# Kernel optimization log

Measured on AMD Instinct MI355X. Metric: run time of the kernel, lower is better.

## Reference

```python
import jax, jax.numpy as jnp
import numpy as np

B = 4096          # events
L = 524288        # total set points (avg 128 per event)
CIN = 16          # per-point feature size (set feature 'a')
DVEC = 32         # flat feature size (feature 'b')
PHI = [128, 128, 64]
MLP = [256, 128]
EPS = 1e-5        # BatchNorm1d eps


def setup_inputs() -> dict:
    key = jax.random.key(0)
    ks = jax.random.split(key, 10)
    def n(k, shape, scale=0.05):
        return jax.random.normal(k, shape, dtype=jnp.float32) * scale
    return {
        "x_a": jax.random.normal(ks[0], (1, CIN, L), dtype=jnp.float32),
        "x_b": jax.random.normal(ks[1], (B, DVEC), dtype=jnp.float32),
        # row 0 -> counts for set feature 'a'; row 1 ignored (Reshape branch)
        "sample_indices": jnp.full((2, B), L // B, dtype=jnp.int32),
        "W1": n(ks[2], (PHI[0], CIN)),  "b1": jnp.zeros((PHI[0],), jnp.float32),
        "W2": n(ks[3], (PHI[1], PHI[0])), "b2": jnp.zeros((PHI[1],), jnp.float32),
        "W3": n(ks[4], (PHI[2], PHI[1])), "b3": jnp.zeros((PHI[2],), jnp.float32),
        "Wm1": n(ks[5], (MLP[0], PHI[2] + DVEC)), "bm1": jnp.zeros((MLP[0],), jnp.float32),
        "g1": jnp.ones((MLP[0],), jnp.float32), "be1": jnp.zeros((MLP[0],), jnp.float32),
        "Wm2": n(ks[6], (MLP[1], MLP[0])), "bm2": jnp.zeros((MLP[1],), jnp.float32),
        "g2": jnp.ones((MLP[1],), jnp.float32), "be2": jnp.zeros((MLP[1],), jnp.float32),
        "Wm3": n(ks[7], (1, MLP[1])), "bm3": jnp.zeros((1,), jnp.float32),
    }


def _bn(x, g, b):
    # BatchNorm1d, training-mode batch stats, biased variance (torch semantics)
    mu = jnp.mean(x, axis=0)
    var = jnp.var(x, axis=0)
    return (x - mu) * jax.lax.rsqrt(var + EPS) * g + b


def reference(x_a, x_b, sample_indices,
              W1, b1, W2, b2, W3, b3,
              Wm1, bm1, g1, be1, Wm2, bm2, g2, be2, Wm3, bm3):
    counts = sample_indices[0].astype(jnp.int32)                       # [B]
    bounds = jnp.concatenate([jnp.zeros((1,), jnp.int32), jnp.cumsum(counts)])  # [B+1]

    # PhiNet: pointwise Conv1d stack (kernel size 1) on [CIN, L]
    h = x_a[0]
    h = jax.nn.relu(jnp.einsum('oc,cl->ol', W1, h) + b1[:, None])
    h = jax.nn.relu(jnp.einsum('oc,cl->ol', W2, h) + b2[:, None])
    h = jax.nn.relu(jnp.einsum('oc,cl->ol', W3, h) + b3[:, None])      # [64, L]

    # fused segment-mean: point p belongs to segment j iff bounds[j] <= p < bounds[j+1]
    seg = jnp.searchsorted(bounds, jnp.arange(h.shape[1], dtype=jnp.int32), side='right') - 1
    sums = jax.ops.segment_sum(h.T, seg, num_segments=counts.shape[0])  # [B, 64]
    means = sums / jnp.maximum(counts, 1).astype(jnp.float32)[:, None]

    # feature order: sorted keys -> ('a' set repr, 'b' flat)
    z = jnp.concatenate([means, x_b.reshape(-1, DVEC)], axis=1)        # [B, 96]

    z = jax.nn.relu(_bn(z @ Wm1.T + bm1, g1, be1))
    z = jax.nn.relu(_bn(z @ Wm2.T + bm2, g2, be2))
    return jax.nn.sigmoid(z @ Wm3.T + bm3)                             # [B, 1]
```

## Files before the change

kernel.cpp:

```cpp
#include <hip/hip_runtime.h>
#include <hip/hip_bf16.h>

#define B_EVENTS 4096
#define L_PTS    524288
#define CIN      16
#define C1       128
#define C2       128
#define C3       64
#define DVEC     32
#define ZDIM     96
#define M1       256
#define M2       128
#define BN_EPS   1e-5f
#define TPTS     64
#define EPB      4

typedef __attribute__((ext_vector_type(8))) short bf16x8;
typedef __attribute__((ext_vector_type(4))) float f32x4;

__device__ __forceinline__ ushort f2bf(float x) {
    union { float f; unsigned u; } a; a.f = x;
    unsigned r = (a.u + 0x7fffu + ((a.u >> 16) & 1u)) >> 16;
    return (ushort)r;
}

__device__ __forceinline__ unsigned cvtpk(float lo, float hi) {
    unsigned r;
    asm("v_cvt_pk_bf16_f32 %0, %1, %2" : "=v"(r) : "v"(lo), "v"(hi));
    return r;
}

__device__ __forceinline__ unsigned long long pack4relu(f32x4 a) {
    union { unsigned u[2]; unsigned long long ll; } pk;
    pk.u[0] = cvtpk(fmaxf(a[0], 0.f), fmaxf(a[1], 0.f));
    pk.u[1] = cvtpk(fmaxf(a[2], 0.f), fmaxf(a[3], 0.f));
    return pk.ll;
}

__device__ __forceinline__ int ldsoff(int base, int rowSlots, int c, int sir) {
    int s = c * rowSlots + sir;
    s ^= (c & 7);
    return base + s * 16;
}

__global__ __launch_bounds__(1024) void scan_zero_kernel(const int* __restrict__ si,
                                                         int* __restrict__ bounds,
                                                         float* __restrict__ stats) {
    __shared__ int sh[1024];
    const int tid = threadIdx.x;
    const int c0 = si[tid*4+0], c1 = si[tid*4+1], c2 = si[tid*4+2], c3 = si[tid*4+3];
    const int s4 = c0 + c1 + c2 + c3;
    sh[tid] = s4;
    if (tid < 768) stats[tid] = 0.f;
    __syncthreads();
    for (int off = 1; off < 1024; off <<= 1) {
        int add = (tid >= off) ? sh[tid - off] : 0;
        __syncthreads();
        sh[tid] += add;
        __syncthreads();
    }
    const int excl = (tid == 0) ? 0 : sh[tid - 1];
    bounds[tid*4+0] = excl;
    bounds[tid*4+1] = excl + c0;
    bounds[tid*4+2] = excl + c0 + c1;
    bounds[tid*4+3] = excl + c0 + c1 + c2;
    if (tid == 1023) bounds[B_EVENTS] = excl + s4;
}

__global__ __launch_bounds__(256) void prep_kernel(
    const float* __restrict__ W1, const float* __restrict__ W2, const float* __restrict__ W3,
    ushort* __restrict__ w1p, ushort* __restrict__ w2b, ushort* __restrict__ w3b)
{
    const int tid = blockIdx.x * 256 + threadIdx.x;
    const int nthr = gridDim.x * 256;
    for (int i = tid; i < C1 * 32; i += nthr) {
        const int r = i >> 5, k = i & 31;
        w1p[i] = (k < CIN) ? f2bf(W1[r * CIN + k]) : (ushort)0;
    }
    for (int i = tid; i < C2 * C1; i += nthr) w2b[i] = f2bf(W2[i]);
    for (int i = tid; i < C3 * C2; i += nthr) w3b[i] = f2bf(W3[i]);
}

__global__ __launch_bounds__(256, 2) void phi_mfma_kernel(
    const float* __restrict__ xa, const float* __restrict__ xb,
    const int* __restrict__ bounds,
    const ushort* __restrict__ w1p, const ushort* __restrict__ w2b, const ushort* __restrict__ w3b,
    const float* __restrict__ b1, const float* __restrict__ b2, const float* __restrict__ b3,
    float* __restrict__ z)
{
    __shared__ __align__(16) char lds[36864];
    __shared__ float msum[C3];

    const int tid  = threadIdx.x;
    const int lane = tid & 63;
    const int wid  = tid >> 6;
    const int wm   = wid >> 1;
    const int wn   = wid & 1;
    const int g4   = lane >> 4;
    const int c16  = lane & 15;

    bf16x8 a1[4], a2[4][4], a3[2][4];
    {
        const int r1 = wm * 64 + c16;
        #pragma unroll
        for (int mf = 0; mf < 4; ++mf)
            a1[mf] = *(const bf16x8*)&w1p[(r1 + mf * 16) * 32 + g4 * 8];
        #pragma unroll
        for (int mf = 0; mf < 4; ++mf)
            #pragma unroll
            for (int kf = 0; kf < 4; ++kf)
                a2[mf][kf] = *(const bf16x8*)&w2b[(r1 + mf * 16) * C1 + kf * 32 + g4 * 8];
        const int r3 = wm * 32 + c16;
        #pragma unroll
        for (int mf = 0; mf < 2; ++mf)
            #pragma unroll
            for (int kf = 0; kf < 4; ++kf)
                a3[mf][kf] = *(const bf16x8*)&w3b[(r3 + mf * 16) * C2 + kf * 32 + g4 * 8];
    }

    const int pt   = tid & 63;
    const int half = tid >> 6;
    const int xoff = ldsoff(0, 4, pt, half >> 1) + (half & 1) * 8;

    for (int e = 0; e < EPB; ++e) {
        const int j     = blockIdx.x * EPB + e;
        const int start = bounds[j];
        const int cnt   = bounds[j + 1] - start;

        if (tid < C3) msum[tid] = 0.f;

        float xr[4];
        #pragma unroll
        for (int jj = 0; jj < 4; ++jj)
            xr[jj] = (pt < cnt) ? xa[(size_t)(half * 4 + jj) * L_PTS + start + pt] : 0.f;
        {
            union { unsigned u[2]; unsigned long long ll; } pk;
            pk.u[0] = cvtpk(xr[0], xr[1]);
            pk.u[1] = cvtpk(xr[2], xr[3]);
            *(unsigned long long*)(lds + xoff) = pk.ll;
        }
        __syncthreads();

        for (int p0 = 0; p0 < cnt; p0 += TPTS) {
            const bool more = (p0 + TPTS) < cnt;

            if (more) {
                const int p = p0 + TPTS + pt;
                #pragma unroll
                for (int jj = 0; jj < 4; ++jj)
                    xr[jj] = (p < cnt) ? xa[(size_t)(half * 4 + jj) * L_PTS + start + p] : 0.f;
            }

            {
                f32x4 acc[4][2];
                #pragma unroll
                for (int mf = 0; mf < 4; ++mf) {
                    const f32x4 bb = *(const f32x4*)&b1[wm * 64 + mf * 16 + g4 * 4];
                    acc[mf][0] = bb; acc[mf][1] = bb;
                }
                bf16x8 bfrag[2];
                #pragma unroll
                for (int nf = 0; nf < 2; ++nf)
                    bfrag[nf] = *(const bf16x8*)(lds + ldsoff(0, 4, wn * 32 + nf * 16 + c16, g4));
                __builtin_amdgcn_s_setprio(1);
                #pragma unroll
                for (int nf = 0; nf < 2; ++nf)
                    #pragma unroll
                    for (int mf = 0; mf < 4; ++mf)
                        acc[mf][nf] = __builtin_amdgcn_mfma_f32_16x16x32_bf16(a1[mf], bfrag[nf], acc[mf][nf], 0, 0, 0);
                __builtin_amdgcn_s_setprio(0);
                #pragma unroll
                for (int mf = 0; mf < 4; ++mf)
                    #pragma unroll
                    for (int nf = 0; nf < 2; ++nf) {
                        const int c = wn * 32 + nf * 16 + c16;
                        const int sir = (wm * 64 + mf * 16) / 8 + (g4 >> 1);
                        *(unsigned long long*)(lds + ldsoff(4096, 16, c, sir) + (g4 & 1) * 8) = pack4relu(acc[mf][nf]);
                    }
            }
            __syncthreads();

            {
                f32x4 acc[4][2];
                #pragma unroll
                for (int mf = 0; mf < 4; ++mf) {
                    const f32x4 bb = *(const f32x4*)&b2[wm * 64 + mf * 16 + g4 * 4];
                    acc[mf][0] = bb; acc[mf][1] = bb;
                }
                #pragma unroll
                for (int nf = 0; nf < 2; ++nf) {
                    const int c = wn * 32 + nf * 16 + c16;
                    bf16x8 bk[4];
                    #pragma unroll
                    for (int kf = 0; kf < 4; ++kf)
                        bk[kf] = *(const bf16x8*)(lds + ldsoff(4096, 16, c, kf * 4 + g4));
                    __builtin_amdgcn_s_setprio(1);
                    #pragma unroll
                    for (int mf = 0; mf < 4; ++mf)
                        #pragma unroll
                        for (int kf = 0; kf < 4; ++kf)
                            acc[mf][nf] = __builtin_amdgcn_mfma_f32_16x16x32_bf16(a2[mf][kf], bk[kf], acc[mf][nf], 0, 0, 0);
                    __builtin_amdgcn_s_setprio(0);
                }
                #pragma unroll
                for (int mf = 0; mf < 4; ++mf)
                    #pragma unroll
                    for (int nf = 0; nf < 2; ++nf) {
                        const int c = wn * 32 + nf * 16 + c16;
                        const int sir = (wm * 64 + mf * 16) / 8 + (g4 >> 1);
                        *(unsigned long long*)(lds + ldsoff(20480, 16, c, sir) + (g4 & 1) * 8) = pack4relu(acc[mf][nf]);
                    }
            }
            __syncthreads();

            if (more) {
                union { unsigned u[2]; unsigned long long ll; } pk;
                pk.u[0] = cvtpk(xr[0], xr[1]);
                pk.u[1] = cvtpk(xr[2], xr[3]);
                *(unsigned long long*)(lds + xoff) = pk.ll;
            }

            {
                f32x4 acc3[2][2];
                #pragma unroll
                for (int mf = 0; mf < 2; ++mf) {
                    const f32x4 bb = *(const f32x4*)&b3[wm * 32 + mf * 16 + g4 * 4];
                    acc3[mf][0] = bb; acc3[mf][1] = bb;
                }
                #pragma unroll
                for (int nf = 0; nf < 2; ++nf) {
                    const int c = wn * 32 + nf * 16 + c16;
                    bf16x8 bk[4];
                    #pragma unroll
                    for (int kf = 0; kf < 4; ++kf)
                        bk[kf] = *(const bf16x8*)(lds + ldsoff(20480, 16, c, kf * 4 + g4));
                    __builtin_amdgcn_s_setprio(1);
                    #pragma unroll
                    for (int mf = 0; mf < 2; ++mf)
                        #pragma unroll
                        for (int kf = 0; kf < 4; ++kf)
                            acc3[mf][nf] = __builtin_amdgcn_mfma_f32_16x16x32_bf16(a3[mf][kf], bk[kf], acc3[mf][nf], 0, 0, 0);
                    __builtin_amdgcn_s_setprio(0);
                }
                float s[2][4];
                #pragma unroll
                for (int mf = 0; mf < 2; ++mf)
                    #pragma unroll
                    for (int r = 0; r < 4; ++r) s[mf][r] = 0.f;
                #pragma unroll
                for (int nf = 0; nf < 2; ++nf) {
                    const int col = p0 + wn * 32 + nf * 16 + c16;
                    const bool valid = col < cnt;
                    #pragma unroll
                    for (int mf = 0; mf < 2; ++mf)
                        #pragma unroll
                        for (int r = 0; r < 4; ++r) {
                            const float v = fmaxf(acc3[mf][nf][r], 0.f);
                            if (valid) s[mf][r] += v;
                        }
                }
                #pragma unroll
                for (int mf = 0; mf < 2; ++mf)
                    #pragma unroll
                    for (int r = 0; r < 4; ++r) {
                        float v = s[mf][r];
                        #pragma unroll
                        for (int m = 1; m < 16; m <<= 1) v += __shfl_xor(v, m, 64);
                        s[mf][r] = v;
                    }
                if (c16 == 0) {
                    #pragma unroll
                    for (int mf = 0; mf < 2; ++mf)
                        #pragma unroll
                        for (int r = 0; r < 4; ++r)
                            atomicAdd(&msum[wm * 32 + mf * 16 + g4 * 4 + r], s[mf][r]);
                }
            }
            __syncthreads();
        }

        if (tid < C3) {
            const float inv = 1.f / (float)max(cnt, 1);
            z[(size_t)j * ZDIM + tid] = msum[tid] * inv;
        } else if (tid < ZDIM) {
            z[(size_t)j * ZDIM + tid] = xb[(size_t)j * DVEC + (tid - C3)];
        }
    }
}

__global__ __launch_bounds__(256) void mlp1_kernel(
    const float* __restrict__ z, const float* __restrict__ Wm1, const float* __restrict__ bm1,
    float* __restrict__ y1, float* __restrict__ gsum, float* __restrict__ gsq)
{
    __shared__ float zs[16][ZDIM + 4];
    const int r0 = blockIdx.x * 16;
    const int tid = threadIdx.x;
    for (int i = tid; i < 16 * ZDIM; i += 256) {
        const int r = i / ZDIM, c = i - r * ZDIM;
        zs[r][c] = z[(size_t)(r0 + r) * ZDIM + c];
    }
    __syncthreads();
    const int o = tid;
    float acc[16];
    const float bb = bm1[o];
    #pragma unroll
    for (int r = 0; r < 16; ++r) acc[r] = bb;
    for (int c = 0; c < ZDIM; c += 4) {
        const float4 w = *(const float4*)&Wm1[o * ZDIM + c];
        #pragma unroll
        for (int r = 0; r < 16; ++r) {
            const float4 v = *(const float4*)&zs[r][c];
            acc[r] += w.x*v.x + w.y*v.y + w.z*v.z + w.w*v.w;
        }
    }
    float s = 0.f, sq = 0.f;
    #pragma unroll
    for (int r = 0; r < 16; ++r) {
        y1[(size_t)(r0 + r) * M1 + o] = acc[r];
        s += acc[r]; sq += acc[r] * acc[r];
    }
    atomicAdd(&gsum[o], s);
    atomicAdd(&gsq[o], sq);
}

__global__ void bnfin_kernel(const float* __restrict__ gsum, const float* __restrict__ gsq,
                             const float* __restrict__ g, const float* __restrict__ be,
                             float* __restrict__ scale, float* __restrict__ shift, int n)
{
    const int o = blockIdx.x * blockDim.x + threadIdx.x;
    if (o >= n) return;
    const float mu  = gsum[o] * (1.f / B_EVENTS);
    const float var = gsq[o] * (1.f / B_EVENTS) - mu * mu;
    const float rs  = rsqrtf(var + BN_EPS);
    const float sc  = rs * g[o];
    scale[o] = sc;
    shift[o] = be[o] - mu * sc;
}

__global__ __launch_bounds__(256) void mlp2_kernel(
    const float* __restrict__ y1, const float* __restrict__ scale1, const float* __restrict__ shift1,
    const float* __restrict__ Wm2, const float* __restrict__ bm2,
    float* __restrict__ y2, float* __restrict__ gsum, float* __restrict__ gsq)
{
    __shared__ float zs[16][M1 + 4];
    const int r0 = blockIdx.x * 16;
    const int tid = threadIdx.x;
    for (int i = tid; i < 16 * M1; i += 256) {
        const int r = i >> 8, c = i & (M1 - 1);
        const float v = y1[(size_t)(r0 + r) * M1 + c];
        zs[r][c] = fmaxf(v * scale1[c] + shift1[c], 0.f);
    }
    __syncthreads();
    const int o = tid & 127;
    const int h = tid >> 7;
    float acc[8];
    const float bb = bm2[o];
    #pragma unroll
    for (int r = 0; r < 8; ++r) acc[r] = bb;
    for (int c = 0; c < M1; c += 4) {
        const float4 w = *(const float4*)&Wm2[o * M1 + c];
        #pragma unroll
        for (int r = 0; r < 8; ++r) {
            const float4 v = *(const float4*)&zs[h * 8 + r][c];
            acc[r] += w.x*v.x + w.y*v.y + w.z*v.z + w.w*v.w;
        }
    }
    float s = 0.f, sq = 0.f;
    #pragma unroll
    for (int r = 0; r < 8; ++r) {
        y2[(size_t)(r0 + h * 8 + r) * M2 + o] = acc[r];
        s += acc[r]; sq += acc[r] * acc[r];
    }
    atomicAdd(&gsum[o], s);
    atomicAdd(&gsq[o], sq);
}

__global__ __launch_bounds__(256) void final_kernel(
    const float* __restrict__ y2, const float* __restrict__ scale2, const float* __restrict__ shift2,
    const float* __restrict__ Wm3, const float* __restrict__ bm3,
    float* __restrict__ out)
{
    const int tid = threadIdx.x;
    const int w = tid >> 6, l = tid & 63;
    const int r = blockIdx.x * 4 + w;
    const float e0 = fmaxf(y2[(size_t)r * M2 + l]      * scale2[l]      + shift2[l],      0.f);
    const float e1 = fmaxf(y2[(size_t)r * M2 + 64 + l] * scale2[64 + l] + shift2[64 + l], 0.f);
    float a = e0 * Wm3[l] + e1 * Wm3[64 + l];
    #pragma unroll
    for (int off = 32; off >= 1; off >>= 1) a += __shfl_down(a, off, 64);
    if (l == 0) out[r] = 1.f / (1.f + expf(-(a + bm3[0])));
}

extern "C" void kernel_launch(void* const* d_in, const int* in_sizes, int n_in,
                              void* d_out, int out_size, void* d_ws, size_t ws_size,
                              hipStream_t stream) {
    const float* xa  = (const float*)d_in[0];
    const float* xb  = (const float*)d_in[1];
    const int*   si  = (const int*)  d_in[2];
    const float* W1  = (const float*)d_in[3];
    const float* b1  = (const float*)d_in[4];
    const float* W2  = (const float*)d_in[5];
    const float* b2  = (const float*)d_in[6];
    const float* W3  = (const float*)d_in[7];
    const float* b3  = (const float*)d_in[8];
    const float* Wm1 = (const float*)d_in[9];
    const float* bm1 = (const float*)d_in[10];
    const float* g1  = (const float*)d_in[11];
    const float* be1 = (const float*)d_in[12];
    const float* Wm2 = (const float*)d_in[13];
    const float* bm2 = (const float*)d_in[14];
    const float* g2  = (const float*)d_in[15];
    const float* be2 = (const float*)d_in[16];
    const float* Wm3 = (const float*)d_in[17];
    const float* bm3 = (const float*)d_in[18];
    float* out = (float*)d_out;

    char* ws = (char*)d_ws;
    size_t off = 0;
    auto alloc = [&](size_t bytes) -> void* {
        void* p = ws + off;
        off = (off + bytes + 255) & ~(size_t)255;
        return p;
    };
    int*    bounds = (int*)   alloc((B_EVENTS + 1) * sizeof(int));
    float*  stats  = (float*) alloc(768 * sizeof(float));
    float*  z      = (float*) alloc((size_t)B_EVENTS * ZDIM * sizeof(float));
    float*  y1     = (float*) alloc((size_t)B_EVENTS * M1 * sizeof(float));
    float*  y2     = (float*) alloc((size_t)B_EVENTS * M2 * sizeof(float));
    float*  scale1 = (float*) alloc(M1 * sizeof(float));
    float*  shift1 = (float*) alloc(M1 * sizeof(float));
    float*  scale2 = (float*) alloc(M2 * sizeof(float));
    float*  shift2 = (float*) alloc(M2 * sizeof(float));
    ushort* w1p    = (ushort*)alloc(C1 * 32 * sizeof(ushort));
    ushort* w2b    = (ushort*)alloc(C2 * C1 * sizeof(ushort));
    ushort* w3b    = (ushort*)alloc(C3 * C2 * sizeof(ushort));
    float* gsum1 = stats;
    float* gsq1  = stats + 256;
    float* gsum2 = stats + 512;
    float* gsq2  = stats + 640;

    hipLaunchKernelGGL(scan_zero_kernel, dim3(1), dim3(1024), 0, stream, si, bounds, stats);
    hipLaunchKernelGGL(prep_kernel, dim3(16), dim3(256), 0, stream, W1, W2, W3, w1p, w2b, w3b);
    hipLaunchKernelGGL(phi_mfma_kernel, dim3(B_EVENTS / EPB), dim3(256), 0, stream,
                       xa, xb, bounds, w1p, w2b, w3b, b1, b2, b3, z);
    hipLaunchKernelGGL(mlp1_kernel, dim3(B_EVENTS / 16), dim3(256), 0, stream,
                       z, Wm1, bm1, y1, gsum1, gsq1);
    hipLaunchKernelGGL(bnfin_kernel, dim3(1), dim3(256), 0, stream,
                       gsum1, gsq1, g1, be1, scale1, shift1, M1);
    hipLaunchKernelGGL(mlp2_kernel, dim3(B_EVENTS / 16), dim3(256), 0, stream,
                       y1, scale1, shift1, Wm2, bm2, y2, gsum2, gsq2);
    hipLaunchKernelGGL(bnfin_kernel, dim3(1), dim3(128), 0, stream,
                       gsum2, gsq2, g2, be2, scale2, shift2, M2);
    hipLaunchKernelGGL(final_kernel, dim3(B_EVENTS / 4), dim3(256), 0, stream,
                       y2, scale2, shift2, Wm3, bm3, out);
}
```

Baseline: 132.8 us.

## Halve phi block to two waves, merge scan and prep, shrink MLP row tiles

Phi blocks now use 128 threads (two waves), each handling 32 points per tile, and process two events per block instead of four. This drops the wn split and halves LDS use, so more blocks are in flight and more workgroups are launched. The scan and weight-prep kernels are merged into one launch, which removes a kernel launch. The MLP kernels handle 8 rows per block instead of 16, which doubles the grid and the number of atomic updates to the BN statistics. Each MFMA tile now covers 32 points, which may lower MFMA efficiency per synchronization.

```diff
diff --git a/kernel.cpp b/kernel.cpp
--- a/kernel.cpp
+++ b/kernel.cpp
@@ -12,8 +12,8 @@
 #define M1       256
 #define M2       128
 #define BN_EPS   1e-5f
-#define TPTS     64
-#define EPB      4
+#define TPTS     32
+#define EPB      2
 
 typedef __attribute__((ext_vector_type(8))) short bf16x8;
 typedef __attribute__((ext_vector_type(4))) float f32x4;
@@ -43,59 +43,56 @@
     return base + s * 16;
 }
 
-__global__ __launch_bounds__(1024) void scan_zero_kernel(const int* __restrict__ si,
-                                                         int* __restrict__ bounds,
-                                                         float* __restrict__ stats) {
-    __shared__ int sh[1024];
-    const int tid = threadIdx.x;
-    const int c0 = si[tid*4+0], c1 = si[tid*4+1], c2 = si[tid*4+2], c3 = si[tid*4+3];
-    const int s4 = c0 + c1 + c2 + c3;
-    sh[tid] = s4;
-    if (tid < 768) stats[tid] = 0.f;
-    __syncthreads();
-    for (int off = 1; off < 1024; off <<= 1) {
-        int add = (tid >= off) ? sh[tid - off] : 0;
-        __syncthreads();
-        sh[tid] += add;
-        __syncthreads();
-    }
-    const int excl = (tid == 0) ? 0 : sh[tid - 1];
-    bounds[tid*4+0] = excl;
-    bounds[tid*4+1] = excl + c0;
-    bounds[tid*4+2] = excl + c0 + c1;
-    bounds[tid*4+3] = excl + c0 + c1 + c2;
-    if (tid == 1023) bounds[B_EVENTS] = excl + s4;
-}
-
-__global__ __launch_bounds__(256) void prep_kernel(
+__global__ __launch_bounds__(1024) void scanprep_kernel(
+    const int* __restrict__ si, int* __restrict__ bounds, float* __restrict__ stats,
     const float* __restrict__ W1, const float* __restrict__ W2, const float* __restrict__ W3,
     ushort* __restrict__ w1p, ushort* __restrict__ w2b, ushort* __restrict__ w3b)
 {
-    const int tid = blockIdx.x * 256 + threadIdx.x;
-    const int nthr = gridDim.x * 256;
-    for (int i = tid; i < C1 * 32; i += nthr) {
-        const int r = i >> 5, k = i & 31;
-        w1p[i] = (k < CIN) ? f2bf(W1[r * CIN + k]) : (ushort)0;
-    }
-    for (int i = tid; i < C2 * C1; i += nthr) w2b[i] = f2bf(W2[i]);
-    for (int i = tid; i < C3 * C2; i += nthr) w3b[i] = f2bf(W3[i]);
-}
-
-__global__ __launch_bounds__(256, 2) void phi_mfma_kernel(
+    if (blockIdx.x == 0) {
+        __shared__ int sh[1024];
+        const int tid = threadIdx.x;
+        const int c0 = si[tid*4+0], c1 = si[tid*4+1], c2 = si[tid*4+2], c3 = si[tid*4+3];
+        const int s4 = c0 + c1 + c2 + c3;
+        sh[tid] = s4;
+        if (tid < 768) stats[tid] = 0.f;
+        __syncthreads();
+        for (int off = 1; off < 1024; off <<= 1) {
+            int add = (tid >= off) ? sh[tid - off] : 0;
+            __syncthreads();
+            sh[tid] += add;
+            __syncthreads();
+        }
+        const int excl = (tid == 0) ? 0 : sh[tid - 1];
+        bounds[tid*4+0] = excl;
+        bounds[tid*4+1] = excl + c0;
+        bounds[tid*4+2] = excl + c0 + c1;
+        bounds[tid*4+3] = excl + c0 + c1 + c2;
+        if (tid == 1023) bounds[B_EVENTS] = excl + s4;
+    } else {
+        const int tid = (blockIdx.x - 1) * 1024 + threadIdx.x;
+        const int nthr = 4 * 1024;
+        for (int i = tid; i < C1 * 32; i += nthr) {
+            const int r = i >> 5, k = i & 31;
+            w1p[i] = (k < CIN) ? f2bf(W1[r * CIN + k]) : (ushort)0;
+        }
+        for (int i = tid; i < C2 * C1; i += nthr) w2b[i] = f2bf(W2[i]);
+        for (int i = tid; i < C3 * C2; i += nthr) w3b[i] = f2bf(W3[i]);
+    }
+}
+
+__global__ __launch_bounds__(128, 2) void phi_mfma_kernel(
     const float* __restrict__ xa, const float* __restrict__ xb,
     const int* __restrict__ bounds,
     const ushort* __restrict__ w1p, const ushort* __restrict__ w2b, const ushort* __restrict__ w3b,
     const float* __restrict__ b1, const float* __restrict__ b2, const float* __restrict__ b3,
     float* __restrict__ z)
 {
-    __shared__ __align__(16) char lds[36864];
+    __shared__ __align__(16) char lds[18432];
     __shared__ float msum[C3];
 
     const int tid  = threadIdx.x;
     const int lane = tid & 63;
-    const int wid  = tid >> 6;
-    const int wm   = wid >> 1;
-    const int wn   = wid & 1;
+    const int wm   = tid >> 6;
     const int g4   = lane >> 4;
     const int c16  = lane & 15;
 
@@ -118,9 +115,9 @@
                 a3[mf][kf] = *(const bf16x8*)&w3b[(r3 + mf * 16) * C2 + kf * 32 + g4 * 8];
     }
 
-    const int pt   = tid & 63;
-    const int half = tid >> 6;
-    const int xoff = ldsoff(0, 4, pt, half >> 1) + (half & 1) * 8;
+    const int pt   = tid & 31;
+    const int qrt  = tid >> 5;
+    const int xoff = ldsoff(0, 4, pt, qrt >> 1) + (qrt & 1) * 8;
 
     for (int e = 0; e < EPB; ++e) {
         const int j     = blockIdx.x * EPB + e;
@@ -132,7 +129,7 @@
         float xr[4];
         #pragma unroll
         for (int jj = 0; jj < 4; ++jj)
-            xr[jj] = (pt < cnt) ? xa[(size_t)(half * 4 + jj) * L_PTS + start + pt] : 0.f;
+            xr[jj] = (pt < cnt) ? xa[(size_t)(qrt * 4 + jj) * L_PTS + start + pt] : 0.f;
         {
             union { unsigned u[2]; unsigned long long ll; } pk;
             pk.u[0] = cvtpk(xr[0], xr[1]);
@@ -148,7 +145,7 @@
                 const int p = p0 + TPTS + pt;
                 #pragma unroll
                 for (int jj = 0; jj < 4; ++jj)
-                    xr[jj] = (p < cnt) ? xa[(size_t)(half * 4 + jj) * L_PTS + start + p] : 0.f;
+                    xr[jj] = (p < cnt) ? xa[(size_t)(qrt * 4 + jj) * L_PTS + start + p] : 0.f;
             }
 
             {
@@ -161,7 +158,7 @@
                 bf16x8 bfrag[2];
                 #pragma unroll
                 for (int nf = 0; nf < 2; ++nf)
-                    bfrag[nf] = *(const bf16x8*)(lds + ldsoff(0, 4, wn * 32 + nf * 16 + c16, g4));
+                    bfrag[nf] = *(const bf16x8*)(lds + ldsoff(0, 4, nf * 16 + c16, g4));
                 __builtin_amdgcn_s_setprio(1);
                 #pragma unroll
                 for (int nf = 0; nf < 2; ++nf)
@@ -173,9 +170,9 @@
                 for (int mf = 0; mf < 4; ++mf)
                     #pragma unroll
                     for (int nf = 0; nf < 2; ++nf) {
-                        const int c = wn * 32 + nf * 16 + c16;
+                        const int c = nf * 16 + c16;
                         const int sir = (wm * 64 + mf * 16) / 8 + (g4 >> 1);
-                        *(unsigned long long*)(lds + ldsoff(4096, 16, c, sir) + (g4 & 1) * 8) = pack4relu(acc[mf][nf]);
+                        *(unsigned long long*)(lds + ldsoff(2048, 16, c, sir) + (g4 & 1) * 8) = pack4relu(acc[mf][nf]);
                     }
             }
             __syncthreads();
@@ -189,11 +186,11 @@
                 }
                 #pragma unroll
                 for (int nf = 0; nf < 2; ++nf) {
-                    const int c = wn * 32 + nf * 16 + c16;
+                    const int c = nf * 16 + c16;
                     bf16x8 bk[4];
                     #pragma unroll
                     for (int kf = 0; kf < 4; ++kf)
-                        bk[kf] = *(const bf16x8*)(lds + ldsoff(4096, 16, c, kf * 4 + g4));
+                        bk[kf] = *(const bf16x8*)(lds + ldsoff(2048, 16, c, kf * 4 + g4));
                     __builtin_amdgcn_s_setprio(1);
                     #pragma unroll
                     for (int mf = 0; mf < 4; ++mf)
@@ -206,9 +203,9 @@
                 for (int mf = 0; mf < 4; ++mf)
                     #pragma unroll
                     for (int nf = 0; nf < 2; ++nf) {
-                        const int c = wn * 32 + nf * 16 + c16;
+                        const int c = nf * 16 + c16;
                         const int sir = (wm * 64 + mf * 16) / 8 + (g4 >> 1);
-                        *(unsigned long long*)(lds + ldsoff(20480, 16, c, sir) + (g4 & 1) * 8) = pack4relu(acc[mf][nf]);
+                        *(unsigned long long*)(lds + ldsoff(10240, 16, c, sir) + (g4 & 1) * 8) = pack4relu(acc[mf][nf]);
                     }
             }
             __syncthreads();
@@ -229,11 +226,11 @@
                 }
                 #pragma unroll
                 for (int nf = 0; nf < 2; ++nf) {
-                    const int c = wn * 32 + nf * 16 + c16;
+                    const int c = nf * 16 + c16;
                     bf16x8 bk[4];
                     #pragma unroll
                     for (int kf = 0; kf < 4; ++kf)
-                        bk[kf] = *(const bf16x8*)(lds + ldsoff(20480, 16, c, kf * 4 + g4));
+                        bk[kf] = *(const bf16x8*)(lds + ldsoff(10240, 16, c, kf * 4 + g4));
                     __builtin_amdgcn_s_setprio(1);
                     #pragma unroll
                     for (int mf = 0; mf < 2; ++mf)
@@ -249,7 +246,7 @@
                     for (int r = 0; r < 4; ++r) s[mf][r] = 0.f;
                 #pragma unroll
                 for (int nf = 0; nf < 2; ++nf) {
-                    const int col = p0 + wn * 32 + nf * 16 + c16;
+                    const int col = p0 + nf * 16 + c16;
                     const bool valid = col < cnt;
                     #pragma unroll
                     for (int mf = 0; mf < 2; ++mf)
@@ -292,30 +289,30 @@
     const float* __restrict__ z, const float* __restrict__ Wm1, const float* __restrict__ bm1,
     float* __restrict__ y1, float* __restrict__ gsum, float* __restrict__ gsq)
 {
-    __shared__ float zs[16][ZDIM + 4];
-    const int r0 = blockIdx.x * 16;
+    __shared__ float zs[8][ZDIM + 4];
+    const int r0 = blockIdx.x * 8;
     const int tid = threadIdx.x;
-    for (int i = tid; i < 16 * ZDIM; i += 256) {
+    for (int i = tid; i < 8 * ZDIM; i += 256) {
         const int r = i / ZDIM, c = i - r * ZDIM;
         zs[r][c] = z[(size_t)(r0 + r) * ZDIM + c];
     }
     __syncthreads();
     const int o = tid;
-    float acc[16];
+    float acc[8];
     const float bb = bm1[o];
     #pragma unroll
-    for (int r = 0; r < 16; ++r) acc[r] = bb;
+    for (int r = 0; r < 8; ++r) acc[r] = bb;
     for (int c = 0; c < ZDIM; c += 4) {
         const float4 w = *(const float4*)&Wm1[o * ZDIM + c];
         #pragma unroll
-        for (int r = 0; r < 16; ++r) {
+        for (int r = 0; r < 8; ++r) {
             const float4 v = *(const float4*)&zs[r][c];
             acc[r] += w.x*v.x + w.y*v.y + w.z*v.z + w.w*v.w;
         }
     }
     float s = 0.f, sq = 0.f;
     #pragma unroll
-    for (int r = 0; r < 16; ++r) {
+    for (int r = 0; r < 8; ++r) {
         y1[(size_t)(r0 + r) * M1 + o] = acc[r];
         s += acc[r]; sq += acc[r] * acc[r];
     }
@@ -342,10 +339,10 @@
     const float* __restrict__ Wm2, const float* __restrict__ bm2,
     float* __restrict__ y2, float* __restrict__ gsum, float* __restrict__ gsq)
 {
-    __shared__ float zs[16][M1 + 4];
-    const int r0 = blockIdx.x * 16;
+    __shared__ float zs[8][M1 + 4];
+    const int r0 = blockIdx.x * 8;
     const int tid = threadIdx.x;
-    for (int i = tid; i < 16 * M1; i += 256) {
+    for (int i = tid; i < 8 * M1; i += 256) {
         const int r = i >> 8, c = i & (M1 - 1);
         const float v = y1[(size_t)(r0 + r) * M1 + c];
         zs[r][c] = fmaxf(v * scale1[c] + shift1[c], 0.f);
@@ -353,22 +350,22 @@
     __syncthreads();
     const int o = tid & 127;
     const int h = tid >> 7;
-    float acc[8];
+    float acc[4];
     const float bb = bm2[o];
     #pragma unroll
-    for (int r = 0; r < 8; ++r) acc[r] = bb;
+    for (int r = 0; r < 4; ++r) acc[r] = bb;
     for (int c = 0; c < M1; c += 4) {
         const float4 w = *(const float4*)&Wm2[o * M1 + c];
         #pragma unroll
-        for (int r = 0; r < 8; ++r) {
-            const float4 v = *(const float4*)&zs[h * 8 + r][c];
+        for (int r = 0; r < 4; ++r) {
+            const float4 v = *(const float4*)&zs[h * 4 + r][c];
             acc[r] += w.x*v.x + w.y*v.y + w.z*v.z + w.w*v.w;
         }
     }
     float s = 0.f, sq = 0.f;
     #pragma unroll
-    for (int r = 0; r < 8; ++r) {
-        y2[(size_t)(r0 + h * 8 + r) * M2 + o] = acc[r];
+    for (int r = 0; r < 4; ++r) {
+        y2[(size_t)(r0 + h * 4 + r) * M2 + o] = acc[r];
         s += acc[r]; sq += acc[r] * acc[r];
     }
     atomicAdd(&gsum[o], s);
@@ -439,15 +436,15 @@
     float* gsum2 = stats + 512;
     float* gsq2  = stats + 640;
 
-    hipLaunchKernelGGL(scan_zero_kernel, dim3(1), dim3(1024), 0, stream, si, bounds, stats);
-    hipLaunchKernelGGL(prep_kernel, dim3(16), dim3(256), 0, stream, W1, W2, W3, w1p, w2b, w3b);
-    hipLaunchKernelGGL(phi_mfma_kernel, dim3(B_EVENTS / EPB), dim3(256), 0, stream,
+    hipLaunchKernelGGL(scanprep_kernel, dim3(5), dim3(1024), 0, stream,
+                       si, bounds, stats, W1, W2, W3, w1p, w2b, w3b);
+    hipLaunchKernelGGL(phi_mfma_kernel, dim3(B_EVENTS / EPB), dim3(128), 0, stream,
                        xa, xb, bounds, w1p, w2b, w3b, b1, b2, b3, z);
-    hipLaunchKernelGGL(mlp1_kernel, dim3(B_EVENTS / 16), dim3(256), 0, stream,
+    hipLaunchKernelGGL(mlp1_kernel, dim3(B_EVENTS / 8), dim3(256), 0, stream,
                        z, Wm1, bm1, y1, gsum1, gsq1);
     hipLaunchKernelGGL(bnfin_kernel, dim3(1), dim3(256), 0, stream,
                        gsum1, gsq1, g1, be1, scale1, shift1, M1);
-    hipLaunchKernelGGL(mlp2_kernel, dim3(B_EVENTS / 16), dim3(256), 0, stream,
+    hipLaunchKernelGGL(mlp2_kernel, dim3(B_EVENTS / 8), dim3(256), 0, stream,
                        y1, scale1, shift1, Wm2, bm2, y2, gsum2, gsq2);
     hipLaunchKernelGGL(bnfin_kernel, dim3(1), dim3(128), 0, stream,
                        gsum2, gsq2, g2, be2, scale2, shift2, M2);
```

After: 146.9 us. 10.6% more time.
